# Kernel optimization log

Hardware: AMD Instinct MI355X
Metric: run time of the kernel (lower is better)

## Reference

```python
import jax, jax.numpy as jnp
import numpy as np

TEMPERATURE = 8.0  # sqrt(d_k=64)

def setup_inputs() -> dict:
    key = jax.random.key(0)
    ks = jax.random.split(key, 6)
    shape = (16, 2048, 64)  # [batch*heads, seq_len, d_k]
    names = ["q_real", "k_real", "v_real", "q_phase", "k_phase", "v_phase"]
    return {n: jax.random.normal(k, shape, dtype=jnp.float32) for n, k in zip(names, ks)}

def reference(q_real, k_real, v_real, q_phase, k_phase, v_phase):
    # Complex QK^T scores: (q_r + i q_p)(k_r + i k_p)^H-style split used by the module
    attn_real = jnp.einsum('bqd,bkd->bqk', q_real, k_real) - jnp.einsum('bqd,bkd->bqk', q_phase, k_phase)
    attn_phase = jnp.einsum('bqd,bkd->bqk', q_real, k_phase) + jnp.einsum('bqd,bkd->bqk', q_phase, k_real)
    # continue_complex=True path, mask=None, dropout in eval (p effectively 0)
    attn_real = jax.nn.softmax(attn_real / TEMPERATURE, axis=2)
    attn_phase = jax.nn.softmax(attn_phase / TEMPERATURE, axis=2)
    output_real = jnp.einsum('bqk,bkd->bqd', attn_real, v_real) - jnp.einsum('bqk,bkd->bqd', attn_phase, v_phase)
    output_phase = jnp.einsum('bqk,bkd->bqd', attn_real, v_phase) + jnp.einsum('bqk,bkd->bqd', attn_phase, v_real)
    return output_real, output_phase, attn_real
```

## Files before the change

kernel.cpp:

```cpp
#include <hip/hip_runtime.h>
#include <hip/hip_bf16.h>
#include <stdint.h>

#define BATCH 16
#define SEQ   2048
#define DK    64
#define BQ    (BATCH * SEQ)
#define MAT   ((size_t)BQ * DK)

typedef float  f32x4  __attribute__((ext_vector_type(4)));
typedef __bf16 bf16x8 __attribute__((ext_vector_type(8)));
typedef unsigned short u16x8 __attribute__((ext_vector_type(8)));
typedef unsigned short u16x4 __attribute__((ext_vector_type(4)));

#define MFMA16(a, b, c) __builtin_amdgcn_mfma_f32_16x16x32_bf16((a), (b), (c), 0, 0, 0)

#define TILEU 16384

__device__ __forceinline__ unsigned short bfbits(float f) {
  return __builtin_bit_cast(unsigned short, __float2bfloat16(f));
}

__device__ __forceinline__ void cvt_store(unsigned short* dst, f32x4 a, f32x4 c) {
  u16x8 v;
  v[0] = bfbits(a[0]); v[1] = bfbits(a[1]); v[2] = bfbits(a[2]); v[3] = bfbits(a[3]);
  v[4] = bfbits(c[0]); v[5] = bfbits(c[1]); v[6] = bfbits(c[2]); v[7] = bfbits(c[3]);
  *(u16x8*)dst = v;
}

__device__ __forceinline__ void gload16(const unsigned short* g, unsigned short* l) {
  __builtin_amdgcn_global_load_lds(
      (const __attribute__((address_space(1))) void*)g,
      (__attribute__((address_space(3))) void*)l, 16, 0, 0);
}

__global__ __launch_bounds__(256)
void ck_convert(const float* __restrict__ kr, const float* __restrict__ kp,
                const float* __restrict__ vr, const float* __restrict__ vp,
                unsigned short* __restrict__ kv)
{
  __shared__ __align__(16) unsigned short VL[8192];
  const int b = blockIdx.x >> 5, tile = blockIdx.x & 31;
  const int tid = threadIdx.x;
  unsigned short* blk = kv + (size_t)(b * 32 + tile) * TILEU;
  const size_t go = ((size_t)b * SEQ + tile * 64) * DK;

  {
    const int row = tid >> 2, cp = tid & 3, sw = row & 7;
    const int c0 = cp * 2, c1 = cp * 2 + 1;
    const float* gr = kr + go + (size_t)row * DK + cp * 16;
    f32x4 r0 = ((const f32x4*)gr)[0], r1 = ((const f32x4*)gr)[1];
    f32x4 r2 = ((const f32x4*)gr)[2], r3 = ((const f32x4*)gr)[3];
    const float* gp = kp + go + (size_t)row * DK + cp * 16;
    f32x4 p0 = ((const f32x4*)gp)[0], p1 = ((const f32x4*)gp)[1];
    f32x4 p2 = ((const f32x4*)gp)[2], p3 = ((const f32x4*)gp)[3];
    cvt_store(blk + row * 64 + (c0 ^ sw) * 8, r0, r1);
    cvt_store(blk + row * 64 + (c1 ^ sw) * 8, r2, r3);
    cvt_store(blk + 4096 + row * 64 + (c0 ^ sw) * 8, p0, p1);
    cvt_store(blk + 4096 + row * 64 + (c1 ^ sw) * 8, p2, p3);
  }
  {
    const int key = tid & 15, d0 = (tid >> 4) * 4;
    #pragma unroll
    for (int pass = 0; pass < 4; ++pass) {
      const int kk = pass * 16 + key;
      f32x4 a = *(const f32x4*)(vr + go + (size_t)kk * DK + d0);
      f32x4 c = *(const f32x4*)(vp + go + (size_t)kk * DK + d0);
      const int kc = kk >> 3, kl = kk & 7;
      #pragma unroll
      for (int j = 0; j < 4; ++j) {
        const int d = d0 + j;
        VL[d * 64 + (kc ^ (d & 7)) * 8 + kl]        = bfbits(a[j]);
        VL[4096 + d * 64 + (kc ^ (d & 7)) * 8 + kl] = bfbits(c[j]);
      }
    }
  }
  __syncthreads();
  #pragma unroll
  for (int it = 0; it < 4; ++it)
    *(u16x8*)(blk + 8192 + it * 2048 + tid * 8) = *(const u16x8*)(VL + it * 2048 + tid * 8);
}

__global__ __launch_bounds__(256)
void ck_qconv(const float* __restrict__ qr, const float* __restrict__ qp,
              unsigned short* __restrict__ qb)
{
  const size_t i8 = ((size_t)blockIdx.x * 256 + threadIdx.x) * 8;
  const float* src = (i8 < MAT) ? qr : qp;
  const size_t off = (i8 < MAT) ? i8 : i8 - MAT;
  f32x4 a = *(const f32x4*)(src + off);
  f32x4 c = *(const f32x4*)(src + off + 4);
  cvt_store(qb + i8, a, c);
}

__global__ __launch_bounds__(256, 4)
void ck_sums(const unsigned short* __restrict__ qb,
             const unsigned short* __restrict__ kv, float* __restrict__ wsums)
{
  __shared__ __align__(16) unsigned short KT[2][8192];

  const int tid  = threadIdx.x;
  const int wq   = tid >> 6, lane = tid & 63;
  const int lrow = lane & 15, lgrp = lane >> 4;

  const int hw = blockIdx.x;
  const int logical = (hw & 7) * 256 + (hw >> 3);
  const int b = logical >> 7, qtile = (logical >> 2) & 31, slice = logical & 3;

  const int qrow = qtile * 64 + wq * 16 + lrow;
  const size_t qoff = ((size_t)b * SEQ + qrow) * DK;
  bf16x8 aQ0 = __builtin_bit_cast(bf16x8, *(const u16x8*)(qb + qoff + lgrp * 8));
  bf16x8 aQ1 = __builtin_bit_cast(bf16x8, *(const u16x8*)(qb + qoff + 32 + lgrp * 8));
  bf16x8 aQ2 = __builtin_bit_cast(bf16x8, *(const u16x8*)(qb + MAT + qoff + lgrp * 8));
  bf16x8 aQ3 = __builtin_bit_cast(bf16x8, *(const u16x8*)(qb + MAT + qoff + 32 + lgrp * 8));

  auto issue = [&](int tile, int buf) {
    const unsigned short* src = kv + (size_t)(b * 32 + tile) * TILEU;
    #pragma unroll
    for (int c = 0; c < 4; ++c) {
      const int ch = wq * 4 + c;
      gload16(src + ch * 512 + lane * 8, &KT[buf][ch * 512]);
    }
  };

  float lsR[4] = {0.f, 0.f, 0.f, 0.f};
  float lsP[4] = {0.f, 0.f, 0.f, 0.f};

  issue(slice * 8 + 0, 0);
  issue(slice * 8 + 1, 1);
  int cur = 0;
  for (int i = 0; i < 8; ++i) {
    if (i < 7) { asm volatile("s_waitcnt vmcnt(4)" ::: "memory"); }
    else       { asm volatile("s_waitcnt vmcnt(0)" ::: "memory"); }
    __builtin_amdgcn_sched_barrier(0);
    __syncthreads();

    const unsigned short* KB = KT[cur];
    #pragma unroll
    for (int t = 0; t < 4; ++t) {
      const int key16 = t * 16 + lrow;
      const int swk = lrow & 7;
      bf16x8 b0 = __builtin_bit_cast(bf16x8, *(const u16x8*)&KB[key16 * 64 + ((lgrp    ) ^ swk) * 8]);
      bf16x8 b1 = __builtin_bit_cast(bf16x8, *(const u16x8*)&KB[key16 * 64 + ((lgrp + 4) ^ swk) * 8]);
      bf16x8 b2 = __builtin_bit_cast(bf16x8, *(const u16x8*)&KB[4096 + key16 * 64 + ((lgrp    ) ^ swk) * 8]);
      bf16x8 b3 = __builtin_bit_cast(bf16x8, *(const u16x8*)&KB[4096 + key16 * 64 + ((lgrp + 4) ^ swk) * 8]);
      f32x4 t1 = {}, t2 = {}, sp = {};
      t1 = MFMA16(aQ0, b0, t1); t1 = MFMA16(aQ1, b1, t1);
      t2 = MFMA16(aQ2, b2, t2); t2 = MFMA16(aQ3, b3, t2);
      sp = MFMA16(aQ0, b2, sp); sp = MFMA16(aQ1, b3, sp);
      sp = MFMA16(aQ2, b0, sp); sp = MFMA16(aQ3, b1, sp);
      #pragma unroll
      for (int r = 0; r < 4; ++r) {
        lsR[r] += __expf((t1[r] - t2[r]) * 0.125f);
        lsP[r] += __expf(sp[r] * 0.125f);
      }
    }
    __syncthreads();
    if (i + 2 < 8) issue(slice * 8 + i + 2, cur);
    cur ^= 1;
  }

  #pragma unroll
  for (int r = 0; r < 4; ++r) {
    float sR = lsR[r], sP = lsP[r];
    #pragma unroll
    for (int m = 1; m < 16; m <<= 1) {
      sR += __shfl_xor(sR, m, 64);
      sP += __shfl_xor(sP, m, 64);
    }
    if (lrow == 0) {
      const size_t row = (size_t)b * SEQ + qtile * 64 + wq * 16 + lgrp * 4 + r;
      wsums[(size_t)(slice * 2 + 0) * BQ + row] = sR;
      wsums[(size_t)(slice * 2 + 1) * BQ + row] = sP;
    }
  }
}

__global__ __launch_bounds__(256, 4)
void ck_main(const unsigned short* __restrict__ qb,
             const unsigned short* __restrict__ kv,
             const float* __restrict__ wsums, float* __restrict__ wsO,
             float* __restrict__ dout)
{
  __shared__ __align__(16) unsigned short KV[16384];
  __shared__ __align__(16) unsigned short Pr[64][32], Pp[64][32];

  const int tid  = threadIdx.x;
  const int wq   = tid >> 6, lane = tid & 63;
  const int lrow = lane & 15, lgrp = lane >> 4;

  const int hw = blockIdx.x;
  const int logical = (hw & 7) * 128 + (hw >> 3);
  const int b = logical >> 6, qtile = (logical >> 1) & 31, half = logical & 1;

  float* attn = dout + 2 * MAT + ((size_t)b * SEQ + (size_t)qtile * 64) * SEQ;

  const int qrow = qtile * 64 + wq * 16 + lrow;
  const size_t qoff = ((size_t)b * SEQ + qrow) * DK;
  bf16x8 aQ0 = __builtin_bit_cast(bf16x8, *(const u16x8*)(qb + qoff + lgrp * 8));
  bf16x8 aQ1 = __builtin_bit_cast(bf16x8, *(const u16x8*)(qb + qoff + 32 + lgrp * 8));
  bf16x8 aQ2 = __builtin_bit_cast(bf16x8, *(const u16x8*)(qb + MAT + qoff + lgrp * 8));
  bf16x8 aQ3 = __builtin_bit_cast(bf16x8, *(const u16x8*)(qb + MAT + qoff + 32 + lgrp * 8));

  const int qloc = wq * 16 + lgrp * 4;
  float iR[4], iP[4];
  {
    const size_t base = (size_t)b * SEQ + qtile * 64 + qloc;
    #pragma unroll
    for (int r = 0; r < 4; ++r) {
      float sR = 0.f, sP = 0.f;
      #pragma unroll
      for (int z = 0; z < 4; ++z) {
        sR += wsums[(size_t)(z * 2 + 0) * BQ + base + r];
        sP += wsums[(size_t)(z * 2 + 1) * BQ + base + r];
      }
      iR[r] = 1.0f / sR;
      iP[r] = 1.0f / sP;
    }
  }

  const u16x8 SGN = {0x8000, 0x8000, 0x8000, 0x8000, 0x8000, 0x8000, 0x8000, 0x8000};
  f32x4 accR[4] = {}, accP[4] = {};

  for (int i = 0; i < 16; ++i) {
    const int tile = half * 16 + i;
    const int k0 = tile * 64;
    const unsigned short* src = kv + (size_t)(b * 32 + tile) * TILEU;
    __syncthreads();
    #pragma unroll
    for (int c = 0; c < 8; ++c) {
      const int ch = wq * 8 + c;
      gload16(src + ch * 512 + lane * 8, KV + ch * 512);
    }
    asm volatile("s_waitcnt vmcnt(0)" ::: "memory");
    __builtin_amdgcn_sched_barrier(0);
    __syncthreads();

    #pragma unroll
    for (int h = 0; h < 2; ++h) {
      #pragma unroll
      for (int t = 0; t < 2; ++t) {
        const int key16 = (h * 2 + t) * 16 + lrow;
        const int swk = lrow & 7;
        bf16x8 b0 = __builtin_bit_cast(bf16x8, *(const u16x8*)&KV[key16 * 64 + ((lgrp    ) ^ swk) * 8]);
        bf16x8 b1 = __builtin_bit_cast(bf16x8, *(const u16x8*)&KV[key16 * 64 + ((lgrp + 4) ^ swk) * 8]);
        bf16x8 b2 = __builtin_bit_cast(bf16x8, *(const u16x8*)&KV[4096 + key16 * 64 + ((lgrp    ) ^ swk) * 8]);
        bf16x8 b3 = __builtin_bit_cast(bf16x8, *(const u16x8*)&KV[4096 + key16 * 64 + ((lgrp + 4) ^ swk) * 8]);
        f32x4 t1 = {}, t2 = {}, sp = {};
        t1 = MFMA16(aQ0, b0, t1); t1 = MFMA16(aQ1, b1, t1);
        t2 = MFMA16(aQ2, b2, t2); t2 = MFMA16(aQ3, b3, t2);
        sp = MFMA16(aQ0, b2, sp); sp = MFMA16(aQ1, b3, sp);
        sp = MFMA16(aQ2, b0, sp); sp = MFMA16(aQ3, b1, sp);
        #pragma unroll
        for (int r = 0; r < 4; ++r) {
          const float er = __expf((t1[r] - t2[r]) * 0.125f) * iR[r];
          const float ep = __expf(sp[r] * 0.125f) * iP[r];
          const int row = qloc + r, col = t * 16 + lrow;
          const int pc = ((col >> 3) ^ (row & 3)) * 8 + (col & 7);
          Pr[row][pc] = bfbits(er);
          Pp[row][pc] = bfbits(ep);
        }
      }
      {
        const int prow = wq * 16 + lrow;
        u16x8 uar = *(const u16x8*)&Pr[prow][(lgrp ^ (prow & 3)) * 8];
        u16x8 uap = *(const u16x8*)&Pp[prow][(lgrp ^ (prow & 3)) * 8];
        u16x8 uan = uap ^ SGN;
        bf16x8 apr = __builtin_bit_cast(bf16x8, uar);
        bf16x8 app = __builtin_bit_cast(bf16x8, uap);
        bf16x8 apn = __builtin_bit_cast(bf16x8, uan);
        #pragma unroll
        for (int nt = 0; nt < 4; ++nt) {
          const int d = nt * 16 + lrow;
          const int cv = ((h * 4 + lgrp) ^ (d & 7)) * 8;
          bf16x8 bvr = __builtin_bit_cast(bf16x8, *(const u16x8*)&KV[8192  + d * 64 + cv]);
          bf16x8 bvp = __builtin_bit_cast(bf16x8, *(const u16x8*)&KV[12288 + d * 64 + cv]);
          accR[nt] = MFMA16(apr, bvr, accR[nt]);
          accR[nt] = MFMA16(apn, bvp, accR[nt]);
          accP[nt] = MFMA16(apr, bvp, accP[nt]);
          accP[nt] = MFMA16(app, bvr, accP[nt]);
        }
      }
      {
        const int j8 = lane & 7;
        #pragma unroll
        for (int s = 0; s < 2; ++s) {
          const int arow = wq * 16 + s * 8 + (lane >> 3);
          const int pc = (((j8 >> 1) ^ (arow & 3)) * 8) + (j8 & 1) * 4;
          u16x4 ua = *(const u16x4*)&Pr[arow][pc];
          f32x4 fa;
          #pragma unroll
          for (int q = 0; q < 4; ++q)
            fa[q] = __builtin_bit_cast(float, (unsigned)ua[q] << 16);
          float* dst = attn + (size_t)arow * SEQ + k0 + h * 32 + j8 * 4;
          __builtin_nontemporal_store(fa, (f32x4*)dst);
        }
      }
    }
  }

  #pragma unroll
  for (int nt = 0; nt < 4; ++nt) {
    const int d = nt * 16 + lrow;
    #pragma unroll
    for (int r = 0; r < 4; ++r) {
      const size_t o = ((size_t)b * SEQ + qtile * 64 + qloc + r) * DK + d;
      wsO[(size_t)(half * 2 + 0) * MAT + o] = accR[nt][r];
      wsO[(size_t)(half * 2 + 1) * MAT + o] = accP[nt][r];
    }
  }
}

__global__ __launch_bounds__(256)
void ck_combine(const float* __restrict__ wsO, float* __restrict__ dout)
{
  const size_t i = ((size_t)blockIdx.x * 256 + threadIdx.x) * 4;
  f32x4 r = *(const f32x4*)(wsO + i)       + *(const f32x4*)(wsO + 2 * MAT + i);
  f32x4 p = *(const f32x4*)(wsO + MAT + i) + *(const f32x4*)(wsO + 3 * MAT + i);
  __builtin_nontemporal_store(r, (f32x4*)(dout + i));
  __builtin_nontemporal_store(p, (f32x4*)(dout + MAT + i));
}

extern "C" void kernel_launch(void* const* d_in, const int* in_sizes, int n_in,
                              void* d_out, int out_size, void* d_ws, size_t ws_size,
                              hipStream_t stream)
{
  const float* qr = (const float*)d_in[0];
  const float* kr = (const float*)d_in[1];
  const float* vr = (const float*)d_in[2];
  const float* qp = (const float*)d_in[3];
  const float* kp = (const float*)d_in[4];
  const float* vp = (const float*)d_in[5];
  float* out = (float*)d_out;

  unsigned short* kv = (unsigned short*)d_ws;
  unsigned short* qb = (unsigned short*)((char*)d_ws + (16u << 20));
  float* wsums = (float*)((char*)d_ws + (24u << 20));
  float* wsO   = (float*)((char*)d_ws + (25u << 20));

  ck_convert<<<BATCH * 32, 256, 0, stream>>>(kr, kp, vr, vp, kv);
  ck_qconv<<<(unsigned)(2 * MAT / 8 / 256), 256, 0, stream>>>(qr, qp, qb);
  ck_sums<<<4 * 32 * BATCH, 256, 0, stream>>>(qb, kv, wsums);
  ck_main<<<2 * 32 * BATCH, 256, 0, stream>>>(qb, kv, wsums, wsO, out);
  ck_combine<<<(unsigned)(MAT / 4 / 256), 256, 0, stream>>>(wsO, out);
}
```

Baseline: 154.6 us.

## Double-buffer KV tiles in main kernel, drop split-K combine, fuse prep kernels

Merges the K/V and Q conversion kernels into one launch. The main kernel now handles all 32 key tiles per block instead of splitting keys in halves, so the workspace partial outputs and the combine kernel go away and results are written straight to the output. KV tile loads are double-buffered in LDS, with the next tile's global-to-LDS load issued while the current one is computed. In exchange, the grid is halved to 512 blocks, LDS use per block doubles and the occupancy hint drops to 2, which lowers parallelism.

```diff
diff --git a/kernel.cpp b/kernel.cpp
--- a/kernel.cpp
+++ b/kernel.cpp
@@ -35,13 +35,25 @@
 }
 
 __global__ __launch_bounds__(256)
-void ck_convert(const float* __restrict__ kr, const float* __restrict__ kp,
-                const float* __restrict__ vr, const float* __restrict__ vp,
-                unsigned short* __restrict__ kv)
+void ck_prep(const float* __restrict__ kr, const float* __restrict__ kp,
+             const float* __restrict__ vr, const float* __restrict__ vp,
+             const float* __restrict__ qr, const float* __restrict__ qp,
+             unsigned short* __restrict__ kv, unsigned short* __restrict__ qb)
 {
   __shared__ __align__(16) unsigned short VL[8192];
+  const int tid = threadIdx.x;
+
+  if (blockIdx.x >= BATCH * 32) {
+    const size_t i8 = ((size_t)(blockIdx.x - BATCH * 32) * 256 + tid) * 8;
+    const float* src = (i8 < MAT) ? qr : qp;
+    const size_t off = (i8 < MAT) ? i8 : i8 - MAT;
+    f32x4 a = *(const f32x4*)(src + off);
+    f32x4 c = *(const f32x4*)(src + off + 4);
+    cvt_store(qb + i8, a, c);
+    return;
+  }
+
   const int b = blockIdx.x >> 5, tile = blockIdx.x & 31;
-  const int tid = threadIdx.x;
   unsigned short* blk = kv + (size_t)(b * 32 + tile) * TILEU;
   const size_t go = ((size_t)b * SEQ + tile * 64) * DK;
 
@@ -79,18 +91,6 @@
   #pragma unroll
   for (int it = 0; it < 4; ++it)
     *(u16x8*)(blk + 8192 + it * 2048 + tid * 8) = *(const u16x8*)(VL + it * 2048 + tid * 8);
-}
-
-__global__ __launch_bounds__(256)
-void ck_qconv(const float* __restrict__ qr, const float* __restrict__ qp,
-              unsigned short* __restrict__ qb)
-{
-  const size_t i8 = ((size_t)blockIdx.x * 256 + threadIdx.x) * 8;
-  const float* src = (i8 < MAT) ? qr : qp;
-  const size_t off = (i8 < MAT) ? i8 : i8 - MAT;
-  f32x4 a = *(const f32x4*)(src + off);
-  f32x4 c = *(const f32x4*)(src + off + 4);
-  cvt_store(qb + i8, a, c);
 }
 
 __global__ __launch_bounds__(256, 4)
@@ -176,13 +176,12 @@
   }
 }
 
-__global__ __launch_bounds__(256, 4)
+__global__ __launch_bounds__(256, 2)
 void ck_main(const unsigned short* __restrict__ qb,
              const unsigned short* __restrict__ kv,
-             const float* __restrict__ wsums, float* __restrict__ wsO,
-             float* __restrict__ dout)
+             const float* __restrict__ wsums, float* __restrict__ dout)
 {
-  __shared__ __align__(16) unsigned short KV[16384];
+  __shared__ __align__(16) unsigned short KV[2][16384];
   __shared__ __align__(16) unsigned short Pr[64][32], Pp[64][32];
 
   const int tid  = threadIdx.x;
@@ -190,9 +189,11 @@
   const int lrow = lane & 15, lgrp = lane >> 4;
 
   const int hw = blockIdx.x;
-  const int logical = (hw & 7) * 128 + (hw >> 3);
-  const int b = logical >> 6, qtile = (logical >> 1) & 31, half = logical & 1;
-
+  const int logical = (hw & 7) * 64 + (hw >> 3);
+  const int b = logical >> 5, qtile = logical & 31;
+
+  float* outR = dout;
+  float* outP = dout + MAT;
   float* attn = dout + 2 * MAT + ((size_t)b * SEQ + (size_t)qtile * 64) * SEQ;
 
   const int qrow = qtile * 64 + wq * 16 + lrow;
@@ -219,33 +220,39 @@
     }
   }
 
+  auto issue = [&](int tile, int buf) {
+    const unsigned short* src = kv + (size_t)(b * 32 + tile) * TILEU;
+    #pragma unroll
+    for (int c = 0; c < 8; ++c) {
+      const int ch = wq * 8 + c;
+      gload16(src + ch * 512 + lane * 8, &KV[buf][ch * 512]);
+    }
+  };
+
   const u16x8 SGN = {0x8000, 0x8000, 0x8000, 0x8000, 0x8000, 0x8000, 0x8000, 0x8000};
   f32x4 accR[4] = {}, accP[4] = {};
 
-  for (int i = 0; i < 16; ++i) {
-    const int tile = half * 16 + i;
-    const int k0 = tile * 64;
-    const unsigned short* src = kv + (size_t)(b * 32 + tile) * TILEU;
-    __syncthreads();
-    #pragma unroll
-    for (int c = 0; c < 8; ++c) {
-      const int ch = wq * 8 + c;
-      gload16(src + ch * 512 + lane * 8, KV + ch * 512);
-    }
-    asm volatile("s_waitcnt vmcnt(0)" ::: "memory");
+  issue(0, 0);
+  issue(1, 1);
+  int cur = 0;
+  for (int i = 0; i < 32; ++i) {
+    const int k0 = i * 64;
+    if (i < 31) { asm volatile("s_waitcnt vmcnt(8)" ::: "memory"); }
+    else        { asm volatile("s_waitcnt vmcnt(0)" ::: "memory"); }
     __builtin_amdgcn_sched_barrier(0);
     __syncthreads();
 
+    const unsigned short* KB = KV[cur];
     #pragma unroll
     for (int h = 0; h < 2; ++h) {
       #pragma unroll
       for (int t = 0; t < 2; ++t) {
         const int key16 = (h * 2 + t) * 16 + lrow;
         const int swk = lrow & 7;
-        bf16x8 b0 = __builtin_bit_cast(bf16x8, *(const u16x8*)&KV[key16 * 64 + ((lgrp    ) ^ swk) * 8]);
-        bf16x8 b1 = __builtin_bit_cast(bf16x8, *(const u16x8*)&KV[key16 * 64 + ((lgrp + 4) ^ swk) * 8]);
-        bf16x8 b2 = __builtin_bit_cast(bf16x8, *(const u16x8*)&KV[4096 + key16 * 64 + ((lgrp    ) ^ swk) * 8]);
-        bf16x8 b3 = __builtin_bit_cast(bf16x8, *(const u16x8*)&KV[4096 + key16 * 64 + ((lgrp + 4) ^ swk) * 8]);
+        bf16x8 b0 = __builtin_bit_cast(bf16x8, *(const u16x8*)&KB[key16 * 64 + ((lgrp    ) ^ swk) * 8]);
+        bf16x8 b1 = __builtin_bit_cast(bf16x8, *(const u16x8*)&KB[key16 * 64 + ((lgrp + 4) ^ swk) * 8]);
+        bf16x8 b2 = __builtin_bit_cast(bf16x8, *(const u16x8*)&KB[4096 + key16 * 64 + ((lgrp    ) ^ swk) * 8]);
+        bf16x8 b3 = __builtin_bit_cast(bf16x8, *(const u16x8*)&KB[4096 + key16 * 64 + ((lgrp + 4) ^ swk) * 8]);
         f32x4 t1 = {}, t2 = {}, sp = {};
         t1 = MFMA16(aQ0, b0, t1); t1 = MFMA16(aQ1, b1, t1);
         t2 = MFMA16(aQ2, b2, t2); t2 = MFMA16(aQ3, b3, t2);
@@ -273,8 +280,8 @@
         for (int nt = 0; nt < 4; ++nt) {
           const int d = nt * 16 + lrow;
           const int cv = ((h * 4 + lgrp) ^ (d & 7)) * 8;
-          bf16x8 bvr = __builtin_bit_cast(bf16x8, *(const u16x8*)&KV[8192  + d * 64 + cv]);
-          bf16x8 bvp = __builtin_bit_cast(bf16x8, *(const u16x8*)&KV[12288 + d * 64 + cv]);
+          bf16x8 bvr = __builtin_bit_cast(bf16x8, *(const u16x8*)&KB[8192  + d * 64 + cv]);
+          bf16x8 bvp = __builtin_bit_cast(bf16x8, *(const u16x8*)&KB[12288 + d * 64 + cv]);
           accR[nt] = MFMA16(apr, bvr, accR[nt]);
           accR[nt] = MFMA16(apn, bvp, accR[nt]);
           accP[nt] = MFMA16(apr, bvp, accP[nt]);
@@ -297,6 +304,9 @@
         }
       }
     }
+    __syncthreads();
+    if (i + 2 < 32) issue(i + 2, cur);
+    cur ^= 1;
   }
 
   #pragma unroll
@@ -305,20 +315,10 @@
     #pragma unroll
     for (int r = 0; r < 4; ++r) {
       const size_t o = ((size_t)b * SEQ + qtile * 64 + qloc + r) * DK + d;
-      wsO[(size_t)(half * 2 + 0) * MAT + o] = accR[nt][r];
-      wsO[(size_t)(half * 2 + 1) * MAT + o] = accP[nt][r];
-    }
-  }
-}
-
-__global__ __launch_bounds__(256)
-void ck_combine(const float* __restrict__ wsO, float* __restrict__ dout)
-{
-  const size_t i = ((size_t)blockIdx.x * 256 + threadIdx.x) * 4;
-  f32x4 r = *(const f32x4*)(wsO + i)       + *(const f32x4*)(wsO + 2 * MAT + i);
-  f32x4 p = *(const f32x4*)(wsO + MAT + i) + *(const f32x4*)(wsO + 3 * MAT + i);
-  __builtin_nontemporal_store(r, (f32x4*)(dout + i));
-  __builtin_nontemporal_store(p, (f32x4*)(dout + MAT + i));
+      outR[o] = accR[nt][r];
+      outP[o] = accP[nt][r];
+    }
+  }
 }
 
 extern "C" void kernel_launch(void* const* d_in, const int* in_sizes, int n_in,
@@ -336,11 +336,9 @@
   unsigned short* kv = (unsigned short*)d_ws;
   unsigned short* qb = (unsigned short*)((char*)d_ws + (16u << 20));
   float* wsums = (float*)((char*)d_ws + (24u << 20));
-  float* wsO   = (float*)((char*)d_ws + (25u << 20));
-
-  ck_convert<<<BATCH * 32, 256, 0, stream>>>(kr, kp, vr, vp, kv);
-  ck_qconv<<<(unsigned)(2 * MAT / 8 / 256), 256, 0, stream>>>(qr, qp, qb);
+
+  const unsigned qblocks = (unsigned)(2 * MAT / 8 / 256);
+  ck_prep<<<BATCH * 32 + qblocks, 256, 0, stream>>>(kr, kp, vr, vp, qr, qp, kv, qb);
   ck_sums<<<4 * 32 * BATCH, 256, 0, stream>>>(qb, kv, wsums);
-  ck_main<<<2 * 32 * BATCH, 256, 0, stream>>>(qb, kv, wsums, wsO, out);
-  ck_combine<<<(unsigned)(MAT / 4 / 256), 256, 0, stream>>>(wsO, out);
-}
+  ck_main<<<32 * BATCH, 256, 0, stream>>>(qb, kv, wsums, out);
+}
```

After: 149.9 us. -3.0%, faster.
